# Kernel tuning notes

Measured on AMD Instinct MI355X. Metric: run time of the kernel, lower is better.

## Reference

```python
import jax, jax.numpy as jnp
import numpy as np
from jax import lax

B, D = 512, 256
C = 10  # hidden conv channels


def setup_inputs() -> dict:
    key = jax.random.key(0)
    ks = jax.random.split(key, 9)
    x = jax.random.normal(ks[0], (B, D, D), jnp.float32)
    w1 = jax.random.normal(ks[1], (C, 1, 1, 1), jnp.float32) * 0.1   # Conv2d(1,10,1)
    b1 = jax.random.normal(ks[2], (C,), jnp.float32) * 0.01
    w2 = jax.random.normal(ks[3], (1, C, 3, 3), jnp.float32) * 0.05  # Conv2d(10,1,3,1,1)
    b2 = jax.random.normal(ks[4], (1,), jnp.float32) * 0.01
    fc1_w = jax.random.normal(ks[5], (4, D * B), jnp.float32) * (1.0 / np.sqrt(D * B))
    fc1_b = jax.random.normal(ks[6], (4,), jnp.float32) * 0.01
    fc2_w = jax.random.normal(ks[7], (2, 4), jnp.float32) * 0.5
    fc2_b = jax.random.normal(ks[8], (2,), jnp.float32) * 0.01
    return {"x": x, "w1": w1, "b1": b1, "w2": w2, "b2": b2,
            "fc1_w": fc1_w, "fc1_b": fc1_b, "fc2_w": fc2_w, "fc2_b": fc2_b}


def reference(x, w1, b1, w2, b2, fc1_w, fc1_b, fc2_w, fc2_b):
    # edge-to-edge: E[b,i,j] = row_sum(i) + col_sum(j)
    rs = x.sum(axis=-1)          # [B, D]
    cs = x.sum(axis=-2)          # [B, D]
    e = (rs[:, :, None] + cs[:, None, :])[:, None]  # [B, 1, D, D]
    # Conv2d(1, C, 1) == per-pixel scale+bias over channels
    h = jax.nn.relu(e * w1.reshape(1, C, 1, 1) + b1.reshape(1, C, 1, 1))  # [B, C, D, D]
    # convSym: lower-triangular mask each channel
    h = h * jnp.tril(jnp.ones((D, D), jnp.float32))
    # Conv2d(C, 1, 3, stride=1, pad=1)
    y = lax.conv_general_dilated(h, w2, (1, 1), 'SAME',
                                 dimension_numbers=('NCHW', 'OIHW', 'NCHW'))
    y = jax.nn.relu(y + b2.reshape(1, 1, 1, 1))[:, 0]  # [B, D, D]
    # edge-to-vertex: v[b,i] = row_sum + col_sum
    v = y.sum(axis=-1) + y.sum(axis=-2)  # [B, D]
    flat = v.reshape(-1)                  # [B*D]
    hfc = jax.nn.relu(fc1_w @ flat + fc1_b)
    return fc2_w @ hfc + fc2_b            # [2]
```

## Files before the change

kernel.cpp:

```cpp
#include <hip/hip_runtime.h>

#define DD 256
#define BB 512

#define OFF_RS   0
#define OFF_CSP  131072
#define OFF_HFC  655360
#define OFF_SBP  655368
#define OFF_TABP 655384

__device__ __forceinline__ float wave_red(float v) {
#pragma unroll
  for (int off = 32; off > 0; off >>= 1) v += __shfl_down(v, off, 64);
  return v;
}

__global__ void ktab_kernel(const float* __restrict__ w1, const float* __restrict__ b1,
                            const float* __restrict__ w2, float* __restrict__ ws) {
  const int t = threadIdx.x;
  float w1v[10], b1v[10], bp[10];
  int rank[10];
#pragma unroll
  for (int c = 0; c < 10; ++c) { w1v[c] = w1[c]; b1v[c] = b1[c]; bp[c] = -b1v[c] / w1v[c]; }
#pragma unroll
  for (int c = 0; c < 10; ++c) {
    int r = 0;
#pragma unroll
    for (int k = 0; k < 10; ++k)
      r += (bp[k] < bp[c] || (bp[k] == bp[c] && k < c)) ? 1 : 0;
    rank[c] = r;
  }
  if (t < 10) ws[OFF_SBP + rank[t]] = bp[t];
  if (t < 99) {
    const int s = t / 9, tt = t % 9;
    const int dr = tt / 3, kc = tt % 3;
    float A = 0.f, Bv = 0.f;
    for (int c = 0; c < 10; ++c) {
      bool act = (w1v[c] > 0.f) ? (rank[c] < s)
               : ((w1v[c] < 0.f) ? (rank[c] >= s) : (b1v[c] > 0.f));
      if (act) { A += w1v[c] * w2[c * 9 + tt]; Bv += b1v[c] * w2[c * 9 + tt]; }
    }
    ws[OFF_TABP + (s * 3 + kc) * 8 + dr * 2]     = A;
    ws[OFF_TABP + (s * 3 + kc) * 8 + dr * 2 + 1] = Bv;
  }
}

__global__ __launch_bounds__(256) void sum_kernel(const float* __restrict__ x,
                                                  float* __restrict__ ws) {
  const int bq = blockIdx.x;
  const int b = bq >> 2;
  const int q = bq & 3;
  const int tid = threadIdx.x;
  const int lane = tid & 63;
  const int wv = tid >> 6;
  __shared__ float rowp[64][65];
  __shared__ float csl[4][DD];
  __shared__ float segp[4][64];
  float4 cacc = make_float4(0.f, 0.f, 0.f, 0.f);
  const float4* px = (const float4*)(x + ((size_t)b << 16) + ((size_t)(q * 64 + wv * 16) << 8));
#pragma unroll
  for (int r = 0; r < 16; ++r) {
    float4 val = px[r * 64 + lane];
    cacc.x += val.x; cacc.y += val.y; cacc.z += val.z; cacc.w += val.w;
    rowp[wv * 16 + r][lane] = (val.x + val.y) + (val.z + val.w);
  }
  ((float4*)csl[wv])[lane] = cacc;
  __syncthreads();
  {
    const int row = tid & 63, seg = tid >> 6;
    const float* rp = rowp[row] + seg * 16;
    float s = 0.f;
#pragma unroll
    for (int k = 0; k < 16; ++k) s += rp[k];
    segp[seg][row] = s;
  }
  __syncthreads();
  if (tid < 64)
    ws[OFF_RS + b * DD + q * 64 + tid] =
        (segp[0][tid] + segp[1][tid]) + (segp[2][tid] + segp[3][tid]);
  ws[OFF_CSP + bq * DD + tid] =
      (csl[0][tid] + csl[1][tid]) + (csl[2][tid] + csl[3][tid]);
  if (bq == 0 && tid < 4) ws[OFF_HFC + tid] = 0.f;
}

__global__ __launch_bounds__(1024, 8) void conv_kernel(const float* __restrict__ b2p,
                                                       const float* __restrict__ fc1w,
                                                       float* __restrict__ ws) {
  const int b = blockIdx.x;
  const int tid = threadIdx.x;
  const int w = tid >> 6;
  const int lane = tid & 63;
  const int wb = w & 3;
  const int seg = w >> 2;
  const int j = wb * 64 + lane;
  const int r0 = seg * 64;

  __shared__ __align__(16) float tabP[264];
  __shared__ float rs_s[DD];
  __shared__ float cs_s[DD];
  __shared__ float wkT[4][DD];
  __shared__ float sbp_s[10];
  __shared__ float red_s[64];

  if (tid < 256) {
    rs_s[tid] = ws[OFF_RS + b * DD + tid];
  } else if (tid < 512) {
    const int t = tid - 256;
    const float* csp = ws + OFF_CSP + (b * 4) * DD + t;
    cs_s[t] = (csp[0] + csp[DD]) + (csp[2 * DD] + csp[3 * DD]);
  } else if (tid < 768) {
    const int r = tid - 512;
#pragma unroll
    for (int k = 0; k < 4; ++k) wkT[k][r] = fc1w[k * (BB * DD) + b * DD + r];
  } else {
    const int u = tid - 768;
    if (u < 264) tabP[u] = ws[OFF_TABP + u];
    if (u >= 256) {  }
    if (u < 10) sbp_s[u] = ws[OFF_SBP + u];
  }
  if (tid < 8) tabP[256 + tid] = ws[OFF_TABP + 256 + tid];
  __syncthreads();

  float sbpv[10];
#pragma unroll
  for (int k = 0; k < 10; ++k) sbpv[k] = sbp_s[k];
  const float b2v = b2p[0];

  float csr[3], vf[3];
  csr[0] = (j >= 1) ? cs_s[j - 1] : 0.f;
  csr[1] = cs_s[j];
  csr[2] = (j < DD - 1) ? cs_s[j + 1] : 0.f;
  vf[0] = (j >= 1) ? 1.f : 0.f;
  vf[1] = 1.f;
  vf[2] = (j < DD - 1) ? 1.f : 0.f;

  const int istart = (r0 == 0) ? 0 : r0 - 1;
  const int iend = (r0 + 64 == DD) ? DD - 1 : r0 + 64;
  const int ifin = r0 + 1;

  float P = 0.f, Q = 0.f, vcol = 0.f;
  float acc0 = 0.f, acc1 = 0.f, acc2 = 0.f, acc3 = 0.f;

  for (int i = istart; i <= iend; ++i) {
    const float rsv = rs_s[i];
    float R0 = 0.f, R1 = 0.f, R2 = 0.f;
    if (j - 1 <= i) {
#pragma unroll
      for (int kc = 0; kc < 3; ++kc) {
        const float e = rsv + csr[kc];
        int s = 0;
#pragma unroll
        for (int k = 0; k < 10; ++k) s += (sbpv[k] < e) ? 1 : 0;
        const float* tp = tabP + (s * 3 + kc) * 8;
        const float4 ab01 = *(const float4*)tp;
        const float2 ab2  = *(const float2*)(tp + 4);
        const float m = ((j - 1 + kc) <= i) ? vf[kc] : 0.f;
        R0 = fmaf(m, fmaf(ab01.x, e, ab01.y), R0);
        R1 = fmaf(m, fmaf(ab01.z, e, ab01.w), R1);
        R2 = fmaf(m, fmaf(ab2.x, e, ab2.y), R2);
      }
    }
    if (i >= ifin) {
      const float y = fmaxf(P + R2 + b2v, 0.f);
      vcol += y;
      const int r = i - 1;
      acc0 = fmaf(y, wkT[0][r], acc0);
      acc1 = fmaf(y, wkT[1][r], acc1);
      acc2 = fmaf(y, wkT[2][r], acc2);
      acc3 = fmaf(y, wkT[3][r], acc3);
    }
    P = Q + R1;
    Q = R0;
  }
  if (r0 + 64 == DD) {
    const float y = fmaxf(P + b2v, 0.f);
    vcol += y;
    acc0 = fmaf(y, wkT[0][DD - 1], acc0);
    acc1 = fmaf(y, wkT[1][DD - 1], acc1);
    acc2 = fmaf(y, wkT[2][DD - 1], acc2);
    acc3 = fmaf(y, wkT[3][DD - 1], acc3);
  }

  acc0 = fmaf(vcol, wkT[0][j], acc0);
  acc1 = fmaf(vcol, wkT[1][j], acc1);
  acc2 = fmaf(vcol, wkT[2][j], acc2);
  acc3 = fmaf(vcol, wkT[3][j], acc3);

  acc0 = wave_red(acc0); acc1 = wave_red(acc1);
  acc2 = wave_red(acc2); acc3 = wave_red(acc3);
  if (lane == 0) {
    red_s[w * 4 + 0] = acc0; red_s[w * 4 + 1] = acc1;
    red_s[w * 4 + 2] = acc2; red_s[w * 4 + 3] = acc3;
  }
  __syncthreads();
  if (tid < 4) {
    float s = 0.f;
#pragma unroll
    for (int wv = 0; wv < 16; ++wv) s += red_s[wv * 4 + tid];
    atomicAdd(&ws[OFF_HFC + tid], s);
  }
}

__global__ void fc_kernel(const float* __restrict__ fc1b, const float* __restrict__ fc2w,
                          const float* __restrict__ fc2b, const float* __restrict__ ws,
                          float* __restrict__ out) {
  if (threadIdx.x == 0 && blockIdx.x == 0) {
    float o0 = fc2b[0], o1 = fc2b[1];
#pragma unroll
    for (int k = 0; k < 4; ++k) {
      float h = fmaxf(ws[OFF_HFC + k] + fc1b[k], 0.f);
      o0 += fc2w[k] * h;
      o1 += fc2w[4 + k] * h;
    }
    out[0] = o0; out[1] = o1;
  }
}

extern "C" void kernel_launch(void* const* d_in, const int* in_sizes, int n_in,
                              void* d_out, int out_size, void* d_ws, size_t ws_size,
                              hipStream_t stream) {
  const float* x    = (const float*)d_in[0];
  const float* w1   = (const float*)d_in[1];
  const float* b1   = (const float*)d_in[2];
  const float* w2   = (const float*)d_in[3];
  const float* b2   = (const float*)d_in[4];
  const float* fc1w = (const float*)d_in[5];
  const float* fc1b = (const float*)d_in[6];
  const float* fc2w = (const float*)d_in[7];
  const float* fc2b = (const float*)d_in[8];
  float* out = (float*)d_out;
  float* ws  = (float*)d_ws;

  hipLaunchKernelGGL(ktab_kernel, dim3(1), dim3(128), 0, stream, w1, b1, w2, ws);
  hipLaunchKernelGGL(sum_kernel,  dim3(2048), dim3(256), 0, stream, x, ws);
  hipLaunchKernelGGL(conv_kernel, dim3(512), dim3(1024), 0, stream, b2, fc1w, ws);
  hipLaunchKernelGGL(fc_kernel,   dim3(1), dim3(64), 0, stream, fc1b, fc2w, fc2b, ws, out);
}
```

Before: 292.9 us.

## Skip masked upper-triangle tiles, use breakpoint LUT, and rebalance conv waves

```diff
diff --git a/kernel.cpp b/kernel.cpp
--- a/kernel.cpp
+++ b/kernel.cpp
@@ -2,12 +2,14 @@
 
 #define DD 256
 #define BB 512
+#define NL 2048
 
 #define OFF_RS   0
 #define OFF_CSP  131072
 #define OFF_HFC  655360
-#define OFF_SBP  655368
-#define OFF_TABP 655384
+#define OFF_PAR  655368
+#define OFF_TABP 655376
+#define OFF_LUT  655648
 
 __device__ __forceinline__ float wave_red(float v) {
 #pragma unroll
@@ -30,7 +32,14 @@
       r += (bp[k] < bp[c] || (bp[k] == bp[c] && k < c)) ? 1 : 0;
     rank[c] = r;
   }
-  if (t < 10) ws[OFF_SBP + rank[t]] = bp[t];
+  float lo = bp[0], hi = bp[0];
+#pragma unroll
+  for (int c = 1; c < 10; ++c) { lo = fminf(lo, bp[c]); hi = fmaxf(hi, bp[c]); }
+  const float step = (hi - lo) / (float)(NL - 3);
+  if (t == 0) {
+    ws[OFF_PAR]     = (float)(NL - 3) / (hi - lo);
+    ws[OFF_PAR + 1] = 1.0f - lo * ((float)(NL - 3) / (hi - lo));
+  }
   if (t < 99) {
     const int s = t / 9, tt = t % 9;
     const int dr = tt / 3, kc = tt % 3;
@@ -42,6 +51,14 @@
     }
     ws[OFF_TABP + (s * 3 + kc) * 8 + dr * 2]     = A;
     ws[OFF_TABP + (s * 3 + kc) * 8 + dr * 2 + 1] = Bv;
+  }
+  unsigned short* lut = (unsigned short*)(ws + OFF_LUT);
+  for (int k = t; k < NL; k += 256) {
+    const float x = lo + (float)(k - 1) * step;
+    int s = 0;
+#pragma unroll
+    for (int c = 0; c < 10; ++c) s += (bp[c] < x) ? 1 : 0;
+    lut[k] = (unsigned short)(s * 96);
   }
 }
 
@@ -90,18 +107,22 @@
   const int tid = threadIdx.x;
   const int w = tid >> 6;
   const int lane = tid & 63;
-  const int wb = w & 3;
-  const int seg = w >> 2;
+  const int q = w >> 2;
+  const int wb = (w - q) & 3;
+  const int seg = q;
   const int j = wb * 64 + lane;
-  const int r0 = seg * 64;
+  const int jmin = wb * 64;
+  const int r0 = seg * 64, r1 = r0 + 64;
 
   __shared__ __align__(16) float tabP[264];
   __shared__ float rs_s[DD];
   __shared__ float cs_s[DD];
-  __shared__ float wkT[4][DD];
-  __shared__ float sbp_s[10];
+  __shared__ __align__(16) float wkA[DD][4];
+  __shared__ unsigned short lut_s[NL];
+  __shared__ float segsum_s[4][4];
   __shared__ float red_s[64];
 
+  ((unsigned int*)lut_s)[tid] = ((const unsigned int*)(ws + OFF_LUT))[tid];
   if (tid < 256) {
     rs_s[tid] = ws[OFF_RS + b * DD + tid];
   } else if (tid < 512) {
@@ -111,20 +132,26 @@
   } else if (tid < 768) {
     const int r = tid - 512;
 #pragma unroll
-    for (int k = 0; k < 4; ++k) wkT[k][r] = fc1w[k * (BB * DD) + b * DD + r];
+    for (int k = 0; k < 4; ++k) wkA[r][k] = fc1w[k * (BB * DD) + b * DD + r];
   } else {
     const int u = tid - 768;
-    if (u < 264) tabP[u] = ws[OFF_TABP + u];
-    if (u >= 256) {  }
-    if (u < 10) sbp_s[u] = ws[OFF_SBP + u];
+    if (u < 256) tabP[u] = ws[OFF_TABP + u];
   }
   if (tid < 8) tabP[256 + tid] = ws[OFF_TABP + 256 + tid];
   __syncthreads();
-
-  float sbpv[10];
-#pragma unroll
-  for (int k = 0; k < 10; ++k) sbpv[k] = sbp_s[k];
+  if (tid < 16) {
+    const int ss = tid >> 2, k = tid & 3;
+    float s = 0.f;
+#pragma unroll
+    for (int r = 0; r < 64; ++r) s += wkA[ss * 64 + r][k];
+    segsum_s[ss][k] = s;
+  }
+  __syncthreads();
+
+  const float inv_step = ws[OFF_PAR];
+  const float bias = ws[OFF_PAR + 1];
   const float b2v = b2p[0];
+  const float yb = fmaxf(b2v, 0.f);
 
   float csr[3], vf[3];
   csr[0] = (j >= 1) ? cs_s[j - 1] : 0.f;
@@ -134,57 +161,67 @@
   vf[1] = 1.f;
   vf[2] = (j < DD - 1) ? 1.f : 0.f;
 
-  const int istart = (r0 == 0) ? 0 : r0 - 1;
-  const int iend = (r0 + 64 == DD) ? DD - 1 : r0 + 64;
-  const int ifin = r0 + 1;
-
-  float P = 0.f, Q = 0.f, vcol = 0.f;
-  float acc0 = 0.f, acc1 = 0.f, acc2 = 0.f, acc3 = 0.f;
-
-  for (int i = istart; i <= iend; ++i) {
-    const float rsv = rs_s[i];
-    float R0 = 0.f, R1 = 0.f, R2 = 0.f;
-    if (j - 1 <= i) {
-#pragma unroll
-      for (int kc = 0; kc < 3; ++kc) {
-        const float e = rsv + csr[kc];
-        int s = 0;
-#pragma unroll
-        for (int k = 0; k < 10; ++k) s += (sbpv[k] < e) ? 1 : 0;
-        const float* tp = tabP + (s * 3 + kc) * 8;
-        const float4 ab01 = *(const float4*)tp;
-        const float2 ab2  = *(const float2*)(tp + 4);
-        const float m = ((j - 1 + kc) <= i) ? vf[kc] : 0.f;
-        R0 = fmaf(m, fmaf(ab01.x, e, ab01.y), R0);
-        R1 = fmaf(m, fmaf(ab01.z, e, ab01.w), R1);
-        R2 = fmaf(m, fmaf(ab2.x, e, ab2.y), R2);
+  const int nt = min(max(jmin - 2 - r0, 0), 64);
+  const int rfirst = r0 + nt;
+  const int ibeg = (nt > 0) ? rfirst - 1 : ((r0 == 0) ? 0 : r0 - 1);
+  const int iend = (r1 == DD) ? DD - 1 : r1;
+  const int ffrom = rfirst + 1;
+
+  float P = 0.f, Q = 0.f;
+  float vcol = 64.f * yb;
+  float acc0 = yb * segsum_s[seg][0];
+  float acc1 = yb * segsum_s[seg][1];
+  float acc2 = yb * segsum_s[seg][2];
+  float acc3 = yb * segsum_s[seg][3];
+
+  if (rfirst < r1) {
+    for (int i = ibeg; i <= iend; ++i) {
+      const float rsv = rs_s[i];
+      float R0 = 0.f, R1 = 0.f, R2 = 0.f;
+      if (j - 1 <= i) {
+#pragma unroll
+        for (int kc = 0; kc < 3; ++kc) {
+          const float e = rsv + csr[kc];
+          float fx = fmaf(e, inv_step, bias);
+          fx = fminf(fmaxf(fx, 0.f), (float)(NL - 1));
+          const int off = (int)lut_s[(int)fx];
+          const char* tp = (const char*)tabP + (off + kc * 32);
+          const float4 ab01 = *(const float4*)tp;
+          const float2 ab2  = *(const float2*)(tp + 16);
+          const float m = ((j - 1 + kc) <= i) ? vf[kc] : 0.f;
+          R0 = fmaf(m, fmaf(ab01.x, e, ab01.y), R0);
+          R1 = fmaf(m, fmaf(ab01.z, e, ab01.w), R1);
+          R2 = fmaf(m, fmaf(ab2.x, e, ab2.y), R2);
+        }
       }
+      if (i >= ffrom) {
+        const float yd = fmaxf(P + R2 + b2v, 0.f) - yb;
+        vcol += yd;
+        const float4 wkv = *(const float4*)wkA[i - 1];
+        acc0 = fmaf(yd, wkv.x, acc0);
+        acc1 = fmaf(yd, wkv.y, acc1);
+        acc2 = fmaf(yd, wkv.z, acc2);
+        acc3 = fmaf(yd, wkv.w, acc3);
+      }
+      P = Q + R1;
+      Q = R0;
     }
-    if (i >= ifin) {
-      const float y = fmaxf(P + R2 + b2v, 0.f);
-      vcol += y;
-      const int r = i - 1;
-      acc0 = fmaf(y, wkT[0][r], acc0);
-      acc1 = fmaf(y, wkT[1][r], acc1);
-      acc2 = fmaf(y, wkT[2][r], acc2);
-      acc3 = fmaf(y, wkT[3][r], acc3);
-    }
-    P = Q + R1;
-    Q = R0;
-  }
-  if (r0 + 64 == DD) {
-    const float y = fmaxf(P + b2v, 0.f);
-    vcol += y;
-    acc0 = fmaf(y, wkT[0][DD - 1], acc0);
-    acc1 = fmaf(y, wkT[1][DD - 1], acc1);
-    acc2 = fmaf(y, wkT[2][DD - 1], acc2);
-    acc3 = fmaf(y, wkT[3][DD - 1], acc3);
-  }
-
-  acc0 = fmaf(vcol, wkT[0][j], acc0);
-  acc1 = fmaf(vcol, wkT[1][j], acc1);
-  acc2 = fmaf(vcol, wkT[2][j], acc2);
-  acc3 = fmaf(vcol, wkT[3][j], acc3);
+  }
+  if (r1 == DD) {
+    const float yd = fmaxf(P + b2v, 0.f) - yb;
+    vcol += yd;
+    const float4 wkv = *(const float4*)wkA[DD - 1];
+    acc0 = fmaf(yd, wkv.x, acc0);
+    acc1 = fmaf(yd, wkv.y, acc1);
+    acc2 = fmaf(yd, wkv.z, acc2);
+    acc3 = fmaf(yd, wkv.w, acc3);
+  }
+
+  const float4 wkj = *(const float4*)wkA[j];
+  acc0 = fmaf(vcol, wkj.x, acc0);
+  acc1 = fmaf(vcol, wkj.y, acc1);
+  acc2 = fmaf(vcol, wkj.z, acc2);
+  acc3 = fmaf(vcol, wkj.w, acc3);
 
   acc0 = wave_red(acc0); acc1 = wave_red(acc1);
   acc2 = wave_red(acc2); acc3 = wave_red(acc3);
@@ -231,7 +268,7 @@
   float* out = (float*)d_out;
   float* ws  = (float*)d_ws;
 
-  hipLaunchKernelGGL(ktab_kernel, dim3(1), dim3(128), 0, stream, w1, b1, w2, ws);
+  hipLaunchKernelGGL(ktab_kernel, dim3(1), dim3(256), 0, stream, w1, b1, w2, ws);
   hipLaunchKernelGGL(sum_kernel,  dim3(2048), dim3(256), 0, stream, x, ws);
   hipLaunchKernelGGL(conv_kernel, dim3(512), dim3(1024), 0, stream, b2, fc1w, ws);
   hipLaunchKernelGGL(fc_kernel,   dim3(1), dim3(64), 0, stream, fc1b, fc2w, fc2b, ws, out);
```

After: 249.7 us. 14.8% less time.
